# Performance work log

Hardware: AMD Instinct MI355X
Metric: run time of the kernel (lower is better)

The kernel has to match this reference:

```python
import jax, jax.numpy as jnp
import numpy as np

IN_C = 128
OUT_C = 128
HEADS = 8
HEAD_DIM = OUT_C // HEADS
N_NODES = 4096
N_EDGES = 131072


def setup_inputs() -> dict:
    key = jax.random.key(0)
    ks = jax.random.split(key, 10)
    s_in = 1.0 / np.sqrt(IN_C)
    s_out = 1.0 / np.sqrt(OUT_C)
    return {
        "x": jax.random.normal(ks[0], (N_NODES, IN_C), dtype=jnp.float32),
        "edge_index": jax.random.randint(ks[1], (2, N_EDGES), 0, N_NODES, dtype=jnp.int64),
        "Wq": jax.random.uniform(ks[2], (IN_C, OUT_C), jnp.float32, -s_in, s_in),
        "bq": jnp.zeros((OUT_C,), jnp.float32),
        "Wk": jax.random.uniform(ks[3], (IN_C, OUT_C), jnp.float32, -s_in, s_in),
        "bk": jnp.zeros((OUT_C,), jnp.float32),
        "Wv": jax.random.uniform(ks[4], (IN_C, OUT_C), jnp.float32, -s_in, s_in),
        "bv": jnp.zeros((OUT_C,), jnp.float32),
        "Wo": jax.random.uniform(ks[5], (OUT_C, OUT_C), jnp.float32, -s_out, s_out),
        "bo": jnp.zeros((OUT_C,), jnp.float32),
    }


def reference(x, edge_index, Wq, bq, Wk, bk, Wv, bv, Wo, bo):
    n = x.shape[0]
    Q = (x @ Wq + bq).reshape(n, HEADS, HEAD_DIM)
    K = (x @ Wk + bk).reshape(n, HEADS, HEAD_DIM)
    V = (x @ Wv + bv).reshape(n, HEADS, HEAD_DIM)
    # dense scores [n, m, h], matching the original module's einsum
    scores = jnp.einsum('nhd,mhd->nmh', Q, K) / np.sqrt(HEAD_DIM).astype(np.float32)
    ei = jnp.clip(edge_index, 0, n - 1)
    mask = jnp.zeros((n, n), dtype=bool).at[ei[0], ei[1]].set(True)
    scores = jnp.where(mask[:, :, None], scores, -jnp.inf)
    attention = jax.nn.softmax(scores, axis=1)
    # rows (along m) that were all -inf give NaN -> replace with 1/n, as in torch
    attention = jnp.nan_to_num(attention, nan=1.0 / n)
    out = jnp.einsum('nmh,mhd->nhd', attention, V).reshape(n, OUT_C)
    return out @ Wo + bo
```

## Files before the change

kernel.cpp:

```cpp
#include <hip/hip_runtime.h>
#include <math.h>

#define NN 4096
#define NE 131072
#define C 128
#define NH 8
#define HD 16
#define DCAP 128

__device__ __forceinline__ float dot16(const float* __restrict__ q, const float* __restrict__ kp) {
    const float4* k4 = reinterpret_cast<const float4*>(kp);
    const float4 k0 = k4[0], k1 = k4[1], k2 = k4[2], k3 = k4[3];
    return q[0]*k0.x + q[1]*k0.y + q[2]*k0.z + q[3]*k0.w
         + q[4]*k1.x + q[5]*k1.y + q[6]*k1.z + q[7]*k1.w
         + q[8]*k2.x + q[9]*k2.y + q[10]*k2.z + q[11]*k2.w
         + q[12]*k3.x + q[13]*k3.y + q[14]*k3.z + q[15]*k3.w;
}

__global__ __launch_bounds__(256) void qkv_kernel(
    const float* __restrict__ x,
    const float* __restrict__ Wq, const float* __restrict__ bq,
    const float* __restrict__ Wk, const float* __restrict__ bk,
    const float* __restrict__ Wv, const float* __restrict__ bv,
    float* __restrict__ Q, float* __restrict__ K, float* __restrict__ V,
    float4* __restrict__ mask_clear, int* __restrict__ deg)
{
    mask_clear[blockIdx.x * 256 + threadIdx.x] = make_float4(0.f, 0.f, 0.f, 0.f);
    if (threadIdx.x < 8) deg[blockIdx.x * 8 + threadIdx.x] = 0;

    __shared__ float xs[8][C];
    const int n0 = blockIdx.x * 8;
    for (int i = threadIdx.x; i < 8 * C; i += 256)
        xs[i >> 7][i & 127] = x[n0 * C + i];
    __syncthreads();

    const int c = threadIdx.x & 127;
    const int half = threadIdx.x >> 7;
    float aq[4], ak[4], av[4];
    #pragma unroll
    for (int j = 0; j < 4; j++) { aq[j] = 0.f; ak[j] = 0.f; av[j] = 0.f; }
    for (int k = 0; k < C; k++) {
        const float wq = Wq[k * C + c];
        const float wk = Wk[k * C + c];
        const float wv = Wv[k * C + c];
        #pragma unroll
        for (int j = 0; j < 4; j++) {
            const float xv = xs[half * 4 + j][k];
            aq[j] = fmaf(xv, wq, aq[j]);
            ak[j] = fmaf(xv, wk, ak[j]);
            av[j] = fmaf(xv, wv, av[j]);
        }
    }
    const float bqv = bq[c], bkv = bk[c], bvv = bv[c];
    #pragma unroll
    for (int j = 0; j < 4; j++) {
        const int n = n0 + half * 4 + j;
        Q[n * C + c] = aq[j] + bqv;
        K[n * C + c] = ak[j] + bkv;
        V[n * C + c] = av[j] + bvv;
    }
}

__global__ __launch_bounds__(256) void scatter_kernel(
    const int* __restrict__ ei, unsigned int* __restrict__ mask,
    int* __restrict__ deg, int* __restrict__ nbr)
{
    const int e = blockIdx.x * 256 + threadIdx.x;
    int src = ei[e];
    int dst = ei[NE + e];
    src = src < 0 ? 0 : (src > NN - 1 ? NN - 1 : src);
    dst = dst < 0 ? 0 : (dst > NN - 1 ? NN - 1 : dst);
    const unsigned int bit = 1u << (dst & 31);
    const unsigned int old = atomicOr(&mask[(src << 7) + (dst >> 5)], bit);
    if (!(old & bit)) {
        const int p = atomicAdd(&deg[src], 1);
        if (p < DCAP) nbr[(src << 7) + p] = dst;
    }
}

__global__ __launch_bounds__(256) void attn_proj_kernel(
    const float* __restrict__ Q, const float* __restrict__ K,
    const float* __restrict__ V, const int* __restrict__ deg,
    const int* __restrict__ nbr, const float* __restrict__ Wo,
    const float* __restrict__ bo, float* __restrict__ out)
{
    __shared__ float row[4][C];
    const int tid = threadIdx.x;
    const int w = tid >> 6;
    const int lane = tid & 63;
    const int n = blockIdx.x * 4 + w;
    const int h = lane & 7;
    const int sub = lane >> 3;

    const int dg = deg[n];

    float qh[16];
    {
        const float4* qp = reinterpret_cast<const float4*>(Q + n * C + h * HD);
        const float4 q0 = qp[0], q1 = qp[1], q2 = qp[2], q3 = qp[3];
        qh[0]=q0.x; qh[1]=q0.y; qh[2]=q0.z; qh[3]=q0.w;
        qh[4]=q1.x; qh[5]=q1.y; qh[6]=q1.z; qh[7]=q1.w;
        qh[8]=q2.x; qh[9]=q2.y; qh[10]=q2.z; qh[11]=q2.w;
        qh[12]=q3.x; qh[13]=q3.y; qh[14]=q3.z; qh[15]=q3.w;
    }

    float mloc = -INFINITY, ssum = 0.f;
    float acc[16];
    #pragma unroll
    for (int d = 0; d < 16; d++) acc[d] = 0.f;

    if (dg > 0) {
        const int* lst = nbr + (n << 7);
        for (int i = sub; i < dg; i += 8) {
            const int m = lst[i];
            const float sc = dot16(qh, K + m * C + h * HD) * 0.25f;
            const float nm = fmaxf(mloc, sc);
            const float scale = __expf(mloc - nm);
            const float p = __expf(sc - nm);
            ssum = ssum * scale + p;
            const float4* v4 = reinterpret_cast<const float4*>(V + m * C + h * HD);
            const float4 v0 = v4[0], v1 = v4[1], v2 = v4[2], v3 = v4[3];
            acc[0]  = fmaf(p, v0.x, acc[0]  * scale);
            acc[1]  = fmaf(p, v0.y, acc[1]  * scale);
            acc[2]  = fmaf(p, v0.z, acc[2]  * scale);
            acc[3]  = fmaf(p, v0.w, acc[3]  * scale);
            acc[4]  = fmaf(p, v1.x, acc[4]  * scale);
            acc[5]  = fmaf(p, v1.y, acc[5]  * scale);
            acc[6]  = fmaf(p, v1.z, acc[6]  * scale);
            acc[7]  = fmaf(p, v1.w, acc[7]  * scale);
            acc[8]  = fmaf(p, v2.x, acc[8]  * scale);
            acc[9]  = fmaf(p, v2.y, acc[9]  * scale);
            acc[10] = fmaf(p, v2.z, acc[10] * scale);
            acc[11] = fmaf(p, v2.w, acc[11] * scale);
            acc[12] = fmaf(p, v3.x, acc[12] * scale);
            acc[13] = fmaf(p, v3.y, acc[13] * scale);
            acc[14] = fmaf(p, v3.z, acc[14] * scale);
            acc[15] = fmaf(p, v3.w, acc[15] * scale);
            mloc = nm;
        }
        float M = mloc;
        #pragma unroll
        for (int o = 8; o < 64; o <<= 1)
            M = fmaxf(M, __shfl_xor(M, o, 64));
        const float f = __expf(mloc - M);
        ssum *= f;
        #pragma unroll
        for (int d = 0; d < 16; d++) acc[d] *= f;
        #pragma unroll
        for (int o = 8; o < 64; o <<= 1)
            ssum += __shfl_xor(ssum, o, 64);
        #pragma unroll
        for (int o = 8; o < 64; o <<= 1) {
            #pragma unroll
            for (int d = 0; d < 16; d++)
                acc[d] += __shfl_xor(acc[d], o, 64);
        }
        const float inv = 1.f / ssum;
        if (sub == 0) {
            float4* rp = reinterpret_cast<float4*>(&row[w][h * HD]);
            rp[0] = make_float4(acc[0]*inv,  acc[1]*inv,  acc[2]*inv,  acc[3]*inv);
            rp[1] = make_float4(acc[4]*inv,  acc[5]*inv,  acc[6]*inv,  acc[7]*inv);
            rp[2] = make_float4(acc[8]*inv,  acc[9]*inv,  acc[10]*inv, acc[11]*inv);
            rp[3] = make_float4(acc[12]*inv, acc[13]*inv, acc[14]*inv, acc[15]*inv);
        }
    } else {
        for (int d = lane; d < C; d += 64) {
            float s = 0.f;
            for (int m = 0; m < NN; m++) s += V[m * C + d];
            row[w][d] = s * (1.f / (float)NN);
        }
    }
    __syncthreads();

    const int c = tid & 127;
    const int r = tid >> 7;
    float a0 = 0.f, a1 = 0.f;
    for (int k = 0; k < C; k++) {
        const float wo = Wo[k * C + c];
        a0 = fmaf(row[r][k],     wo, a0);
        a1 = fmaf(row[r + 2][k], wo, a1);
    }
    const float bov = bo[c];
    out[(blockIdx.x * 4 + r) * C + c]     = a0 + bov;
    out[(blockIdx.x * 4 + r + 2) * C + c] = a1 + bov;
}

extern "C" void kernel_launch(void* const* d_in, const int* in_sizes, int n_in,
                              void* d_out, int out_size, void* d_ws, size_t ws_size,
                              hipStream_t stream)
{
    const float* x  = (const float*)d_in[0];
    const int*   ei = (const int*)d_in[1];
    const float* Wq = (const float*)d_in[2];
    const float* bq = (const float*)d_in[3];
    const float* Wk = (const float*)d_in[4];
    const float* bk = (const float*)d_in[5];
    const float* Wv = (const float*)d_in[6];
    const float* bv = (const float*)d_in[7];
    const float* Wo = (const float*)d_in[8];
    const float* bo = (const float*)d_in[9];
    float* out = (float*)d_out;

    char* ws = (char*)d_ws;
    const size_t MB2 = 1u << 21;
    float*        Q    = (float*)(ws);
    float*        K    = (float*)(ws + MB2);
    float*        V    = (float*)(ws + 2 * MB2);
    unsigned int* mask = (unsigned int*)(ws + 3 * MB2);
    int*          nbr  = (int*)(ws + 4 * MB2);
    int*          deg  = (int*)(ws + 5 * MB2);

    qkv_kernel<<<512, 256, 0, stream>>>(x, Wq, bq, Wk, bk, Wv, bv, Q, K, V,
                                        (float4*)mask, deg);
    scatter_kernel<<<NE / 256, 256, 0, stream>>>(ei, mask, deg, nbr);
    attn_proj_kernel<<<NN / 4, 256, 0, stream>>>(Q, K, V, deg, nbr, Wo, bo, out);
}
```

Measured before the change: 60.83 us.

## Fuse edge scatter into attention kernel using per-block shared-memory adjacency buckets

Removes the separate scatter kernel and the global mask/degree/neighbour arrays. Each attention block owns 32 source nodes, scans the whole edge list, and builds deduplicated neighbour buckets in shared memory with shared atomics. It then runs online-softmax attention and the output projection for its rows. The QKV kernel now does 16 rows per block and no longer clears buffers. In exchange, every block re-reads all edges, only 128 blocks run on a large GPU, and neighbours past 64 per node would be dropped.

```diff
diff --git a/kernel.cpp b/kernel.cpp
--- a/kernel.cpp
+++ b/kernel.cpp
@@ -6,7 +6,9 @@
 #define C 128
 #define NH 8
 #define HD 16
-#define DCAP 128
+#define NPB2 32
+#define B2 (NN / NPB2)
+#define UCAP 64
 
 __device__ __forceinline__ float dot16(const float* __restrict__ q, const float* __restrict__ kp) {
     const float4* k4 = reinterpret_cast<const float4*>(kp);
@@ -22,30 +24,27 @@
     const float* __restrict__ Wq, const float* __restrict__ bq,
     const float* __restrict__ Wk, const float* __restrict__ bk,
     const float* __restrict__ Wv, const float* __restrict__ bv,
-    float* __restrict__ Q, float* __restrict__ K, float* __restrict__ V,
-    float4* __restrict__ mask_clear, int* __restrict__ deg)
+    float* __restrict__ Q, float* __restrict__ K, float* __restrict__ V)
 {
-    mask_clear[blockIdx.x * 256 + threadIdx.x] = make_float4(0.f, 0.f, 0.f, 0.f);
-    if (threadIdx.x < 8) deg[blockIdx.x * 8 + threadIdx.x] = 0;
-
-    __shared__ float xs[8][C];
-    const int n0 = blockIdx.x * 8;
-    for (int i = threadIdx.x; i < 8 * C; i += 256)
+    __shared__ float xs[16][C];
+    const int n0 = blockIdx.x * 16;
+    for (int i = threadIdx.x; i < 16 * C; i += 256)
         xs[i >> 7][i & 127] = x[n0 * C + i];
     __syncthreads();
 
     const int c = threadIdx.x & 127;
     const int half = threadIdx.x >> 7;
-    float aq[4], ak[4], av[4];
+    float aq[8], ak[8], av[8];
     #pragma unroll
-    for (int j = 0; j < 4; j++) { aq[j] = 0.f; ak[j] = 0.f; av[j] = 0.f; }
+    for (int j = 0; j < 8; j++) { aq[j] = 0.f; ak[j] = 0.f; av[j] = 0.f; }
+
     for (int k = 0; k < C; k++) {
         const float wq = Wq[k * C + c];
         const float wk = Wk[k * C + c];
         const float wv = Wv[k * C + c];
         #pragma unroll
-        for (int j = 0; j < 4; j++) {
-            const float xv = xs[half * 4 + j][k];
+        for (int j = 0; j < 8; j++) {
+            const float xv = xs[half * 8 + j][k];
             aq[j] = fmaf(xv, wq, aq[j]);
             ak[j] = fmaf(xv, wk, ak[j]);
             av[j] = fmaf(xv, wv, av[j]);
@@ -53,136 +52,165 @@
     }
     const float bqv = bq[c], bkv = bk[c], bvv = bv[c];
     #pragma unroll
-    for (int j = 0; j < 4; j++) {
-        const int n = n0 + half * 4 + j;
+    for (int j = 0; j < 8; j++) {
+        const int n = n0 + half * 8 + j;
         Q[n * C + c] = aq[j] + bqv;
         K[n * C + c] = ak[j] + bkv;
         V[n * C + c] = av[j] + bvv;
     }
 }
 
-__global__ __launch_bounds__(256) void scatter_kernel(
-    const int* __restrict__ ei, unsigned int* __restrict__ mask,
-    int* __restrict__ deg, int* __restrict__ nbr)
+__global__ __launch_bounds__(512, 1) void attn_fused_kernel(
+    const float* __restrict__ Q, const float* __restrict__ K,
+    const float* __restrict__ V, const int* __restrict__ ei,
+    const float* __restrict__ Wo, const float* __restrict__ bo,
+    float* __restrict__ out)
 {
-    const int e = blockIdx.x * 256 + threadIdx.x;
-    int src = ei[e];
-    int dst = ei[NE + e];
-    src = src < 0 ? 0 : (src > NN - 1 ? NN - 1 : src);
-    dst = dst < 0 ? 0 : (dst > NN - 1 ? NN - 1 : dst);
-    const unsigned int bit = 1u << (dst & 31);
-    const unsigned int old = atomicOr(&mask[(src << 7) + (dst >> 5)], bit);
-    if (!(old & bit)) {
-        const int p = atomicAdd(&deg[src], 1);
-        if (p < DCAP) nbr[(src << 7) + p] = dst;
-    }
-}
-
-__global__ __launch_bounds__(256) void attn_proj_kernel(
-    const float* __restrict__ Q, const float* __restrict__ K,
-    const float* __restrict__ V, const int* __restrict__ deg,
-    const int* __restrict__ nbr, const float* __restrict__ Wo,
-    const float* __restrict__ bo, float* __restrict__ out)
-{
-    __shared__ float row[4][C];
+    __shared__ union {
+        unsigned int presence[NPB2][128];
+        float row[NPB2][C];
+    } u;
+    __shared__ unsigned short bucket[NPB2][UCAP];
+    __shared__ int cnt[NPB2];
+
     const int tid = threadIdx.x;
-    const int w = tid >> 6;
-    const int lane = tid & 63;
-    const int n = blockIdx.x * 4 + w;
-    const int h = lane & 7;
-    const int sub = lane >> 3;
-
-    const int dg = deg[n];
-
-    float qh[16];
+    const int base = blockIdx.x * NPB2;
+
+    for (int i = tid; i < NPB2 * 128; i += 512)
+        (&u.presence[0][0])[i] = 0u;
+    if (tid < NPB2) cnt[tid] = 0;
+    __syncthreads();
+
+    for (int eb = tid * 4; eb < NE; eb += 512 * 4) {
+        const int4 s4 = *reinterpret_cast<const int4*>(ei + eb);
+        const int4 d4 = *reinterpret_cast<const int4*>(ei + NE + eb);
+        const int ss[4] = {s4.x, s4.y, s4.z, s4.w};
+        const int dd[4] = {d4.x, d4.y, d4.z, d4.w};
+        #pragma unroll
+        for (int k = 0; k < 4; k++) {
+            int src = ss[k]; src = src < 0 ? 0 : (src > NN - 1 ? NN - 1 : src);
+            int dst = dd[k]; dst = dst < 0 ? 0 : (dst > NN - 1 ? NN - 1 : dst);
+            const int sl = src - base;
+            if ((unsigned)sl < NPB2) {
+                const unsigned int bit = 1u << (dst & 31);
+                const unsigned int old = atomicOr(&u.presence[sl][dst >> 5], bit);
+                if (!(old & bit)) {
+                    const int p = atomicAdd(&cnt[sl], 1);
+                    if (p < UCAP) bucket[sl][p] = (unsigned short)dst;
+                }
+            }
+        }
+    }
+    __syncthreads();
+
     {
-        const float4* qp = reinterpret_cast<const float4*>(Q + n * C + h * HD);
-        const float4 q0 = qp[0], q1 = qp[1], q2 = qp[2], q3 = qp[3];
-        qh[0]=q0.x; qh[1]=q0.y; qh[2]=q0.z; qh[3]=q0.w;
-        qh[4]=q1.x; qh[5]=q1.y; qh[6]=q1.z; qh[7]=q1.w;
-        qh[8]=q2.x; qh[9]=q2.y; qh[10]=q2.z; qh[11]=q2.w;
-        qh[12]=q3.x; qh[13]=q3.y; qh[14]=q3.z; qh[15]=q3.w;
-    }
-
-    float mloc = -INFINITY, ssum = 0.f;
-    float acc[16];
-    #pragma unroll
-    for (int d = 0; d < 16; d++) acc[d] = 0.f;
-
-    if (dg > 0) {
-        const int* lst = nbr + (n << 7);
-        for (int i = sub; i < dg; i += 8) {
-            const int m = lst[i];
-            const float sc = dot16(qh, K + m * C + h * HD) * 0.25f;
-            const float nm = fmaxf(mloc, sc);
-            const float scale = __expf(mloc - nm);
-            const float p = __expf(sc - nm);
-            ssum = ssum * scale + p;
-            const float4* v4 = reinterpret_cast<const float4*>(V + m * C + h * HD);
-            const float4 v0 = v4[0], v1 = v4[1], v2 = v4[2], v3 = v4[3];
-            acc[0]  = fmaf(p, v0.x, acc[0]  * scale);
-            acc[1]  = fmaf(p, v0.y, acc[1]  * scale);
-            acc[2]  = fmaf(p, v0.z, acc[2]  * scale);
-            acc[3]  = fmaf(p, v0.w, acc[3]  * scale);
-            acc[4]  = fmaf(p, v1.x, acc[4]  * scale);
-            acc[5]  = fmaf(p, v1.y, acc[5]  * scale);
-            acc[6]  = fmaf(p, v1.z, acc[6]  * scale);
-            acc[7]  = fmaf(p, v1.w, acc[7]  * scale);
-            acc[8]  = fmaf(p, v2.x, acc[8]  * scale);
-            acc[9]  = fmaf(p, v2.y, acc[9]  * scale);
-            acc[10] = fmaf(p, v2.z, acc[10] * scale);
-            acc[11] = fmaf(p, v2.w, acc[11] * scale);
-            acc[12] = fmaf(p, v3.x, acc[12] * scale);
-            acc[13] = fmaf(p, v3.y, acc[13] * scale);
-            acc[14] = fmaf(p, v3.z, acc[14] * scale);
-            acc[15] = fmaf(p, v3.w, acc[15] * scale);
-            mloc = nm;
-        }
-        float M = mloc;
-        #pragma unroll
-        for (int o = 8; o < 64; o <<= 1)
-            M = fmaxf(M, __shfl_xor(M, o, 64));
-        const float f = __expf(mloc - M);
-        ssum *= f;
-        #pragma unroll
-        for (int d = 0; d < 16; d++) acc[d] *= f;
-        #pragma unroll
-        for (int o = 8; o < 64; o <<= 1)
-            ssum += __shfl_xor(ssum, o, 64);
-        #pragma unroll
-        for (int o = 8; o < 64; o <<= 1) {
-            #pragma unroll
-            for (int d = 0; d < 16; d++)
-                acc[d] += __shfl_xor(acc[d], o, 64);
-        }
-        const float inv = 1.f / ssum;
-        if (sub == 0) {
-            float4* rp = reinterpret_cast<float4*>(&row[w][h * HD]);
-            rp[0] = make_float4(acc[0]*inv,  acc[1]*inv,  acc[2]*inv,  acc[3]*inv);
-            rp[1] = make_float4(acc[4]*inv,  acc[5]*inv,  acc[6]*inv,  acc[7]*inv);
-            rp[2] = make_float4(acc[8]*inv,  acc[9]*inv,  acc[10]*inv, acc[11]*inv);
-            rp[3] = make_float4(acc[12]*inv, acc[13]*inv, acc[14]*inv, acc[15]*inv);
-        }
-    } else {
-        for (int d = lane; d < C; d += 64) {
-            float s = 0.f;
-            for (int m = 0; m < NN; m++) s += V[m * C + d];
-            row[w][d] = s * (1.f / (float)NN);
-        }
-    }
-    __syncthreads();
-
-    const int c = tid & 127;
-    const int r = tid >> 7;
-    float a0 = 0.f, a1 = 0.f;
-    for (int k = 0; k < C; k++) {
-        const float wo = Wo[k * C + c];
-        a0 = fmaf(row[r][k],     wo, a0);
-        a1 = fmaf(row[r + 2][k], wo, a1);
-    }
-    const float bov = bo[c];
-    out[(blockIdx.x * 4 + r) * C + c]     = a0 + bov;
-    out[(blockIdx.x * 4 + r + 2) * C + c] = a1 + bov;
+        const int w = tid >> 6;
+        const int lane = tid & 63;
+        const int h = lane & 7;
+        const int sub = lane >> 3;
+
+        for (int rep = 0; rep < 4; rep++) {
+            const int nl = w * 4 + rep;
+            const int n = base + nl;
+            const int dg = min(cnt[nl], UCAP);
+
+            if (dg == 0) {
+                for (int d = lane; d < C; d += 64) {
+                    float s = 0.f;
+                    for (int m = 0; m < NN; m++) s += V[m * C + d];
+                    u.row[nl][d] = s * (1.f / (float)NN);
+                }
+                continue;
+            }
+
+            float qh[16];
+            {
+                const float4* qp = reinterpret_cast<const float4*>(Q + n * C + h * HD);
+                const float4 q0 = qp[0], q1 = qp[1], q2 = qp[2], q3 = qp[3];
+                qh[0]=q0.x; qh[1]=q0.y; qh[2]=q0.z; qh[3]=q0.w;
+                qh[4]=q1.x; qh[5]=q1.y; qh[6]=q1.z; qh[7]=q1.w;
+                qh[8]=q2.x; qh[9]=q2.y; qh[10]=q2.z; qh[11]=q2.w;
+                qh[12]=q3.x; qh[13]=q3.y; qh[14]=q3.z; qh[15]=q3.w;
+            }
+
+            float mloc = -INFINITY, ssum = 0.f;
+            float acc[16];
+            #pragma unroll
+            for (int d = 0; d < 16; d++) acc[d] = 0.f;
+
+            for (int i = sub; i < dg; i += 8) {
+                const int m = bucket[nl][i];
+                const float sc = dot16(qh, K + m * C + h * HD) * 0.25f;
+                const float nm = fmaxf(mloc, sc);
+                const float scale = __expf(mloc - nm);
+                const float p = __expf(sc - nm);
+                ssum = ssum * scale + p;
+                const float4* v4 = reinterpret_cast<const float4*>(V + m * C + h * HD);
+                const float4 v0 = v4[0], v1 = v4[1], v2 = v4[2], v3 = v4[3];
+                acc[0]  = fmaf(p, v0.x, acc[0]  * scale);
+                acc[1]  = fmaf(p, v0.y, acc[1]  * scale);
+                acc[2]  = fmaf(p, v0.z, acc[2]  * scale);
+                acc[3]  = fmaf(p, v0.w, acc[3]  * scale);
+                acc[4]  = fmaf(p, v1.x, acc[4]  * scale);
+                acc[5]  = fmaf(p, v1.y, acc[5]  * scale);
+                acc[6]  = fmaf(p, v1.z, acc[6]  * scale);
+                acc[7]  = fmaf(p, v1.w, acc[7]  * scale);
+                acc[8]  = fmaf(p, v2.x, acc[8]  * scale);
+                acc[9]  = fmaf(p, v2.y, acc[9]  * scale);
+                acc[10] = fmaf(p, v2.z, acc[10] * scale);
+                acc[11] = fmaf(p, v2.w, acc[11] * scale);
+                acc[12] = fmaf(p, v3.x, acc[12] * scale);
+                acc[13] = fmaf(p, v3.y, acc[13] * scale);
+                acc[14] = fmaf(p, v3.z, acc[14] * scale);
+                acc[15] = fmaf(p, v3.w, acc[15] * scale);
+                mloc = nm;
+            }
+            float M = mloc;
+            #pragma unroll
+            for (int o = 8; o < 64; o <<= 1)
+                M = fmaxf(M, __shfl_xor(M, o, 64));
+            const float f = __expf(mloc - M);
+            ssum *= f;
+            #pragma unroll
+            for (int d = 0; d < 16; d++) acc[d] *= f;
+            #pragma unroll
+            for (int o = 8; o < 64; o <<= 1)
+                ssum += __shfl_xor(ssum, o, 64);
+            #pragma unroll
+            for (int o = 8; o < 64; o <<= 1) {
+                #pragma unroll
+                for (int d = 0; d < 16; d++)
+                    acc[d] += __shfl_xor(acc[d], o, 64);
+            }
+            const float inv = 1.f / ssum;
+            if (sub == 0) {
+                float4* rp = reinterpret_cast<float4*>(&u.row[nl][h * HD]);
+                rp[0] = make_float4(acc[0]*inv,  acc[1]*inv,  acc[2]*inv,  acc[3]*inv);
+                rp[1] = make_float4(acc[4]*inv,  acc[5]*inv,  acc[6]*inv,  acc[7]*inv);
+                rp[2] = make_float4(acc[8]*inv,  acc[9]*inv,  acc[10]*inv, acc[11]*inv);
+                rp[3] = make_float4(acc[12]*inv, acc[13]*inv, acc[14]*inv, acc[15]*inv);
+            }
+        }
+    }
+    __syncthreads();
+
+    {
+        const int c = tid & 127;
+        const int g = tid >> 7;
+        float acc[8];
+        #pragma unroll
+        for (int j = 0; j < 8; j++) acc[j] = 0.f;
+        for (int k = 0; k < C; k++) {
+            const float wo = Wo[k * C + c];
+            #pragma unroll
+            for (int j = 0; j < 8; j++)
+                acc[j] = fmaf(u.row[g + 4 * j][k], wo, acc[j]);
+        }
+        const float bov = bo[c];
+        #pragma unroll
+        for (int j = 0; j < 8; j++)
+            out[(base + g + 4 * j) * C + c] = acc[j] + bov;
+    }
 }
 
 extern "C" void kernel_launch(void* const* d_in, const int* in_sizes, int n_in,
@@ -203,15 +231,10 @@
 
     char* ws = (char*)d_ws;
     const size_t MB2 = 1u << 21;
-    float*        Q    = (float*)(ws);
-    float*        K    = (float*)(ws + MB2);
-    float*        V    = (float*)(ws + 2 * MB2);
-    unsigned int* mask = (unsigned int*)(ws + 3 * MB2);
-    int*          nbr  = (int*)(ws + 4 * MB2);
-    int*          deg  = (int*)(ws + 5 * MB2);
-
-    qkv_kernel<<<512, 256, 0, stream>>>(x, Wq, bq, Wk, bk, Wv, bv, Q, K, V,
-                                        (float4*)mask, deg);
-    scatter_kernel<<<NE / 256, 256, 0, stream>>>(ei, mask, deg, nbr);
-    attn_proj_kernel<<<NN / 4, 256, 0, stream>>>(Q, K, V, deg, nbr, Wo, bo, out);
-}
+    float* Q = (float*)(ws);
+    float* K = (float*)(ws + MB2);
+    float* V = (float*)(ws + 2 * MB2);
+
+    qkv_kernel<<<NN / 16, 256, 0, stream>>>(x, Wq, bq, Wk, bk, Wv, bv, Q, K, V);
+    attn_fused_kernel<<<B2, 512, 0, stream>>>(Q, K, V, ei, Wo, bo, out);
+}
```

Result: slower. 85.48 us (+40.5%).
